# Optimization experiments

Measured on AMD Instinct MI355X. Metric: run time of the kernel, lower is better.

The kernel has to match this reference:

```python
import jax, jax.numpy as jnp
import numpy as np

N_NODES = 100000
N_EDGES = 1600000
N_GRAPHS = 128
CONV = [64, 64, 64]
HID = [256, 128, 2]
GFT = 64
EPS = 1e-5
NEG_SLOPE = 0.01


def leaky_relu(x):
    return jnp.where(x >= 0, x, NEG_SLOPE * x)


def setup_inputs() -> dict:
    key = jax.random.key(0)
    ks = jax.random.split(key, 32)
    inp = {}
    inp['x'] = jax.random.normal(ks[0], (N_NODES, CONV[0]), dtype=jnp.float32)
    inp['edge_index'] = jax.random.randint(ks[1], (2, N_EDGES), 0, N_NODES, dtype=jnp.int64)
    inp['graph_features'] = jax.random.normal(ks[2], (N_GRAPHS, GFT), dtype=jnp.float32)
    inp['batch'] = jnp.sort(jax.random.randint(ks[3], (N_NODES,), 0, N_GRAPHS, dtype=jnp.int64))
    # SAGEConv params per layer: W_l (aggregated branch, with bias), W_r (root branch), BN gamma/beta
    ki = 4
    for li in range(len(CONV) - 1):
        fin, fout = CONV[li], CONV[li + 1]
        s = 1.0 / np.sqrt(fin)
        inp[f'Wl{li}'] = jax.random.uniform(ks[ki], (fin, fout), minval=-s, maxval=s); ki += 1
        inp[f'bl{li}'] = jax.random.uniform(ks[ki], (fout,), minval=-s, maxval=s); ki += 1
        inp[f'Wr{li}'] = jax.random.uniform(ks[ki], (fin, fout), minval=-s, maxval=s); ki += 1
        inp[f'g{li}'] = jnp.ones((fout,), jnp.float32)
        inp[f'b{li}'] = jnp.zeros((fout,), jnp.float32)
    # MLP: Linear(128->256), LeakyReLU, Linear(256->128), LeakyReLU, Linear(128->2)
    dims = [CONV[-1] + GFT] + HID
    for li in range(len(HID)):
        fin, fout = dims[li], dims[li + 1]
        s = 1.0 / np.sqrt(fin)
        inp[f'Wm{li}'] = jax.random.uniform(ks[ki], (fin, fout), minval=-s, maxval=s); ki += 1
        inp[f'bm{li}'] = jax.random.uniform(ks[ki], (fout,), minval=-s, maxval=s); ki += 1
    return inp


def _sage_block(x, src, dst, Wl, bl, Wr, gamma, beta):
    # PyG SAGEConv (aggr='mean'): out = lin_l(mean_{j in N(i)} x_j) + lin_r(x_i)
    msgs = x[src]                                               # [E, Fin] gather
    agg = jax.ops.segment_sum(msgs, dst, num_segments=N_NODES)  # [N, Fin] scatter-add
    deg = jax.ops.segment_sum(jnp.ones((src.shape[0],), x.dtype), dst, num_segments=N_NODES)
    agg = agg / jnp.maximum(deg, 1.0)[:, None]
    h = agg @ Wl + bl + x @ Wr
    h = leaky_relu(h)
    # BatchNorm1d (training mode: batch stats over nodes, biased variance)
    mu = h.mean(axis=0)
    var = h.var(axis=0)
    return (h - mu) * jax.lax.rsqrt(var + EPS) * gamma + beta


def reference(x, edge_index, graph_features, batch,
              Wl0, bl0, Wr0, g0, b0, Wl1, bl1, Wr1, g1, b1,
              Wm0, bm0, Wm1, bm1, Wm2, bm2):
    src, dst = edge_index[0], edge_index[1]
    h = _sage_block(x, src, dst, Wl0, bl0, Wr0, g0, b0)
    h = _sage_block(h, src, dst, Wl1, bl1, Wr1, g1, b1)
    # scatter_mean graph pooling
    pooled = jax.ops.segment_sum(h, batch, num_segments=N_GRAPHS)
    cnt = jax.ops.segment_sum(jnp.ones((h.shape[0],), h.dtype), batch, num_segments=N_GRAPHS)
    pooled = pooled / jnp.maximum(cnt, 1.0)[:, None]
    z = jnp.concatenate([pooled, graph_features], axis=1)       # [G, 128]
    z = leaky_relu(z @ Wm0 + bm0)
    z = leaky_relu(z @ Wm1 + bm1)
    return z @ Wm2 + bm2
```

## Files before the change

kernel.cpp:

```cpp
#include <hip/hip_runtime.h>

#define N_NODES 100000
#define N_EDGES 1600000
#define N_GRAPHS 128
#define FDIM 64
#define EPSV 1e-5f
#define NEG 0.01f

#define NB 782
#define PART_BLOCKS 391
#define CVT_BLOCKS 1563
#define NTILES 6250
#define TPB 8
#define GEMM_BLOCKS 782

typedef short bf16x8 __attribute__((ext_vector_type(8)));
typedef float f32x4  __attribute__((ext_vector_type(4)));

__device__ __forceinline__ float leaky(float x){ return x >= 0.f ? x : NEG*x; }

__device__ __forceinline__ unsigned short f2bf(float x){
    unsigned u = __float_as_uint(x);
    return (unsigned short)((u + 0x7fffu + ((u >> 16) & 1u)) >> 16);
}
__device__ __forceinline__ float bf2f(unsigned short b){
    return __uint_as_float(((unsigned)b) << 16);
}

__global__ __launch_bounds__(256) void k_prep(const float* __restrict__ x,
                                              unsigned short* __restrict__ o,
                                              const int* __restrict__ dst,
                                              int* __restrict__ bhist,
                                              float* __restrict__ bnpart){
    __shared__ int lh[NB];
    int b = blockIdx.x, t = threadIdx.x;
    if (b < CVT_BLOCKS){
        int base = b*1024 + t;
        #pragma unroll
        for (int k2 = 0; k2 < 4; ++k2){
            int i = base + k2*256;
            if (i < (N_NODES*FDIM)/4){
                float4 v = ((const float4*)x)[i];
                ushort4 r;
                r.x = f2bf(v.x); r.y = f2bf(v.y); r.z = f2bf(v.z); r.w = f2bf(v.w);
                ((ushort4*)o)[i] = r;
            }
        }
        if (b < 16) bnpart[(b << 8) + t] = 0.f;
    } else {
        for (int i = t; i < NB; i += 256) lh[i] = 0;
        __syncthreads();
        int base = (b - CVT_BLOCKS) * 4096;
        #pragma unroll
        for (int k = 0; k < 16; ++k){
            int e = base + k*256 + t;
            if (e < N_EDGES) atomicAdd(&lh[dst[e] >> 7], 1);
        }
        __syncthreads();
        for (int i = t; i < NB; i += 256) if (lh[i]) atomicAdd(&bhist[i], lh[i]);
    }
}

__global__ __launch_bounds__(256) void k_bscan(const int* __restrict__ bhist,
                                               int* __restrict__ boff, int* __restrict__ cur){
    __shared__ int lds[256];
    int t = threadIdx.x;
    int base = t*4;
    int v0 = (base+0 < NB) ? bhist[base+0] : 0;
    int v1 = (base+1 < NB) ? bhist[base+1] : 0;
    int v2 = (base+2 < NB) ? bhist[base+2] : 0;
    int v3 = (base+3 < NB) ? bhist[base+3] : 0;
    lds[t] = v0+v1+v2+v3; __syncthreads();
    for (int off = 1; off < 256; off <<= 1){
        int add = (t >= off) ? lds[t-off] : 0; __syncthreads();
        lds[t] += add; __syncthreads();
    }
    int excl = (t > 0) ? lds[t-1] : 0;
    int p0 = excl, p1 = excl+v0, p2 = excl+v0+v1, p3 = excl+v0+v1+v2;
    if (base+0 < NB){ boff[base+0] = p0; cur[base+0] = p0; }
    if (base+1 < NB){ boff[base+1] = p1; cur[base+1] = p1; }
    if (base+2 < NB){ boff[base+2] = p2; cur[base+2] = p2; }
    if (base+3 < NB){ boff[base+3] = p3; cur[base+3] = p3; }
    if (t == 0) boff[NB] = N_EDGES;
}

__global__ __launch_bounds__(256) void k_part(const int* __restrict__ src, const int* __restrict__ dst,
                                              int* __restrict__ cur, int* __restrict__ packed){
    __shared__ int lh[NB];
    __shared__ int lc[NB];
    int t = threadIdx.x;
    for (int i = t; i < NB; i += 256) lh[i] = 0;
    __syncthreads();
    int base = blockIdx.x * 4096;
    int d[16];
    #pragma unroll
    for (int k = 0; k < 16; ++k){
        int e = base + k*256 + t;
        d[k] = (e < N_EDGES) ? dst[e] : -1;
        if (d[k] >= 0) atomicAdd(&lh[d[k] >> 7], 1);
    }
    __syncthreads();
    for (int i = t; i < NB; i += 256) lc[i] = atomicAdd(&cur[i], lh[i]);
    __syncthreads();
    #pragma unroll
    for (int k = 0; k < 16; ++k){
        int e = base + k*256 + t;
        if (e < N_EDGES){
            int b = d[k] >> 7;
            int p = atomicAdd(&lc[b], 1);
            packed[p] = (src[e] << 7) | (d[k] & 127);
        }
    }
}

__global__ __launch_bounds__(256) void k_sort(const int* __restrict__ packed,
                                              const int* __restrict__ boff,
                                              int* __restrict__ rs, int* __restrict__ colb){
    __shared__ int hist[128];
    __shared__ int curs[128];
    int b = blockIdx.x, t = threadIdx.x;
    int e0 = boff[b], e1 = boff[b+1];
    if (t < 128) hist[t] = 0;
    __syncthreads();
    for (int e = e0 + t; e < e1; e += 256)
        atomicAdd(&hist[packed[e] & 127], 1);
    __syncthreads();
    int cnt = (t < 128) ? hist[t] : 0;
    __syncthreads();
    for (int off = 1; off < 128; off <<= 1){
        int add = (t < 128 && t >= off) ? hist[t-off] : 0;
        __syncthreads();
        if (t < 128) hist[t] += add;
        __syncthreads();
    }
    int nbase = b << 7;
    int nloc = min(128, N_NODES - nbase);
    if (t < nloc){
        int excl = hist[t] - cnt;
        rs[nbase + t] = e0 + excl;
        curs[t] = excl;
    }
    __syncthreads();
    for (int e = e0 + t; e < e1; e += 256){
        int v = packed[e];
        int p = atomicAdd(&curs[v & 127], 1);
        colb[e0 + p] = v & 0xFFFFFF80;
    }
    if (b == 0 && t == 0) rs[N_NODES] = N_EDGES;
}

template<int PASS>
__global__ __launch_bounds__(256) void k_agg(
    const unsigned short* __restrict__ xin, const int* __restrict__ rs,
    const int* __restrict__ colb, unsigned short* __restrict__ agg)
{
    int t = threadIdx.x;
    int lane = t & 63;
    int sub = lane >> 3;
    int q   = lane & 7;
    const char* xb = (const char*)xin + (PASS << 6) + (q << 3);
    int wid = (blockIdx.x << 2) + (t >> 6);
    const int nw = gridDim.x << 2;
    for (int n = wid; n < N_NODES; n += nw){
        int e0 = __builtin_amdgcn_readfirstlane(rs[n]);
        int e1 = __builtin_amdgcn_readfirstlane(rs[n+1]);
        float ax=0.f, ay=0.f, az=0.f, aw=0.f;
        for (int e = e0 + sub; e < e1; e += 32){
            {
                uint2 u = *(const uint2*)(xb + colb[e]);
                ax += __uint_as_float(u.x << 16); ay += __uint_as_float(u.x & 0xffff0000u);
                az += __uint_as_float(u.y << 16); aw += __uint_as_float(u.y & 0xffff0000u);
            }
            int i1 = e + 8, i2 = e + 16, i3 = e + 24;
            if (i1 < e1){
                uint2 u = *(const uint2*)(xb + colb[i1]);
                ax += __uint_as_float(u.x << 16); ay += __uint_as_float(u.x & 0xffff0000u);
                az += __uint_as_float(u.y << 16); aw += __uint_as_float(u.y & 0xffff0000u);
            }
            if (i2 < e1){
                uint2 u = *(const uint2*)(xb + colb[i2]);
                ax += __uint_as_float(u.x << 16); ay += __uint_as_float(u.x & 0xffff0000u);
                az += __uint_as_float(u.y << 16); aw += __uint_as_float(u.y & 0xffff0000u);
            }
            if (i3 < e1){
                uint2 u = *(const uint2*)(xb + colb[i3]);
                ax += __uint_as_float(u.x << 16); ay += __uint_as_float(u.x & 0xffff0000u);
                az += __uint_as_float(u.y << 16); aw += __uint_as_float(u.y & 0xffff0000u);
            }
        }
        ax += __shfl_xor(ax, 8, 64); ay += __shfl_xor(ay, 8, 64);
        az += __shfl_xor(az, 8, 64); aw += __shfl_xor(aw, 8, 64);
        ax += __shfl_xor(ax, 16, 64); ay += __shfl_xor(ay, 16, 64);
        az += __shfl_xor(az, 16, 64); aw += __shfl_xor(aw, 16, 64);
        ax += __shfl_xor(ax, 32, 64); ay += __shfl_xor(ay, 32, 64);
        az += __shfl_xor(az, 32, 64); aw += __shfl_xor(aw, 32, 64);
        if (sub == 0){
            float rd = 1.f / fmaxf((float)(e1 - e0), 1.f);
            ushort4 o;
            o.x = f2bf(ax*rd); o.y = f2bf(ay*rd);
            o.z = f2bf(az*rd); o.w = f2bf(aw*rd);
            *(ushort4*)((char*)agg + (((size_t)n) << 7) + (PASS << 6) + (q << 3)) = o;
        }
    }
}

template<bool AFF>
__global__ __launch_bounds__(256) void k_gemm(
    const unsigned short* __restrict__ agg,
    const unsigned short* __restrict__ xin,
    unsigned short* __restrict__ hout,
    const int* __restrict__ rs, const int* __restrict__ batch,
    const float* __restrict__ Wl, const float* __restrict__ Wr,
    const float* __restrict__ scale,
    const float* __restrict__ bbias, const float* __restrict__ bdelta,
    float* __restrict__ bnpart, float* __restrict__ S)
{
    __shared__ float sS[8*64];
    int t = threadIdx.x;
    int lane = t & 63;
    int jt = t >> 6;
    int g = lane >> 4, r = lane & 15;
    int j = (jt << 4) + r;

    bf16x8 wlh[2], wll[2], wrh[2], wrl[2];
    #pragma unroll
    for (int ks = 0; ks < 2; ++ks){
        #pragma unroll
        for (int i = 0; i < 8; ++i){
            int k = (ks << 5) + (g << 3) + i;
            float s = AFF ? scale[k] : 1.f;
            float wv = Wl[(k << 6) + j] * s;
            unsigned u = __float_as_uint(wv);
            wlh[ks][i] = (short)(u >> 16);
            float lf = wv - __uint_as_float(u & 0xffff0000u);
            wll[ks][i] = (short)(__float_as_uint(lf) >> 16);
            wv = Wr[(k << 6) + j] * s;
            u = __float_as_uint(wv);
            wrh[ks][i] = (short)(u >> 16);
            lf = wv - __uint_as_float(u & 0xffff0000u);
            wrl[ks][i] = (short)(__float_as_uint(lf) >> 16);
        }
    }

    float bb = bbias[j];
    float bd = AFF ? bdelta[j] : 0.f;

    int gbase = 0, span = 0;
    if (AFF){
        for (int i = t; i < 512; i += 256) sS[i] = 0.f;
        int nfirst = blockIdx.x * (TPB*16);
        int nlast  = min(nfirst + TPB*16 - 1, N_NODES - 1);
        gbase = batch[nfirst];
        span  = batch[nlast] - gbase + 1;
        __syncthreads();
    }

    float bs = 0.f, bq = 0.f;
    int c0 = blockIdx.x * TPB;
    int cend = min(c0 + TPB, NTILES);

    auto LOADT = [&](int tile, bf16x8* A, bf16x8* X, int4& R, int& R5, int4& B){
        size_t rowoff = (((size_t)((tile << 4) + r)) << 6) + (g << 3);
        const bf16x8* pa = (const bf16x8*)(agg + rowoff);
        const bf16x8* px = (const bf16x8*)(xin + rowoff);
        A[0] = pa[0]; A[1] = pa[4];
        X[0] = px[0]; X[1] = px[4];
        if (AFF){
            int nb = (tile << 4) + (g << 2);
            R  = *(const int4*)(rs + nb);
            R5 = rs[nb + 4];
            B  = *(const int4*)(batch + nb);
        }
    };

    auto POOL = [&](int gr, float hv){
        int lg = gr - gbase;
        if (lg < 8) atomicAdd(&sS[(lg << 6) + j], hv);
        else        atomicAdd(&S[(gr << 6) + j], hv);
    };

    auto COMPUTE = [&](int tile, const bf16x8* A, const bf16x8* X,
                       const int4& R, int R5, const int4& B){
        f32x4 accA = {0.f, 0.f, 0.f, 0.f};
        f32x4 accX = {0.f, 0.f, 0.f, 0.f};
        accA = __builtin_amdgcn_mfma_f32_16x16x32_bf16(A[0], wlh[0], accA, 0, 0, 0);
        accA = __builtin_amdgcn_mfma_f32_16x16x32_bf16(A[0], wll[0], accA, 0, 0, 0);
        accA = __builtin_amdgcn_mfma_f32_16x16x32_bf16(A[1], wlh[1], accA, 0, 0, 0);
        accA = __builtin_amdgcn_mfma_f32_16x16x32_bf16(A[1], wll[1], accA, 0, 0, 0);
        accX = __builtin_amdgcn_mfma_f32_16x16x32_bf16(X[0], wrh[0], accX, 0, 0, 0);
        accX = __builtin_amdgcn_mfma_f32_16x16x32_bf16(X[0], wrl[0], accX, 0, 0, 0);
        accX = __builtin_amdgcn_mfma_f32_16x16x32_bf16(X[1], wrh[1], accX, 0, 0, 0);
        accX = __builtin_amdgcn_mfma_f32_16x16x32_bf16(X[1], wrl[1], accX, 0, 0, 0);

        int nb = (tile << 4) + (g << 2);
        if (AFF){
            float hv;
            hv = accA[0] + accX[0] + bb + ((R.y - R.x) > 0 ? bd : 0.f);
            hv = leaky(hv); bs += hv; bq += hv*hv; POOL(B.x, hv);
            hv = accA[1] + accX[1] + bb + ((R.z - R.y) > 0 ? bd : 0.f);
            hv = leaky(hv); bs += hv; bq += hv*hv; POOL(B.y, hv);
            hv = accA[2] + accX[2] + bb + ((R.w - R.z) > 0 ? bd : 0.f);
            hv = leaky(hv); bs += hv; bq += hv*hv; POOL(B.z, hv);
            hv = accA[3] + accX[3] + bb + ((R5 - R.w) > 0 ? bd : 0.f);
            hv = leaky(hv); bs += hv; bq += hv*hv; POOL(B.w, hv);
        } else {
            #pragma unroll
            for (int q = 0; q < 4; ++q){
                float hv = leaky(accA[q] + accX[q] + bb);
                unsigned short h16 = f2bf(hv);
                float hr = bf2f(h16);
                hout[((size_t)(nb + q) << 6) + j] = h16;
                bs += hr; bq += hr*hr;
            }
        }
    };

    bf16x8 Aa[2], Xa[2], Ab[2], Xb[2];
    int4 Ra = {0,0,0,0}, Rb = {0,0,0,0}, Ba = {0,0,0,0}, Bb = {0,0,0,0};
    int R5a = 0, R5b = 0;

    LOADT(c0, Aa, Xa, Ra, R5a, Ba);
    for (int c = c0; c < cend; c += 2){
        if (c + 1 < cend) LOADT(c + 1, Ab, Xb, Rb, R5b, Bb);
        COMPUTE(c, Aa, Xa, Ra, R5a, Ba);
        if (c + 2 < cend) LOADT(c + 2, Aa, Xa, Ra, R5a, Ba);
        if (c + 1 < cend) COMPUTE(c + 1, Ab, Xb, Rb, R5b, Bb);
    }

    bs += __shfl_xor(bs, 16, 64); bs += __shfl_xor(bs, 32, 64);
    bq += __shfl_xor(bq, 16, 64); bq += __shfl_xor(bq, 32, 64);
    if (lane < 16){
        float* bp = bnpart + ((blockIdx.x & 31) * 128);
        atomicAdd(&bp[(jt << 4) + lane], bs);
        atomicAdd(&bp[64 + (jt << 4) + lane], bq);
    }

    if (AFF){
        __syncthreads();
        int sp = min(span, 8);
        for (int i = t; i < (sp << 6); i += 256){
            float v = sS[i];
            if (v != 0.f) atomicAdd(&S[((gbase + (i >> 6)) << 6) + (i & 63)], v);
        }
    }
}

template<bool FOLD>
__global__ __launch_bounds__(64) void k_bnfin(
    float* __restrict__ bnpart,
    const float* __restrict__ gamma, const float* __restrict__ beta,
    const float* __restrict__ Wl_nx, const float* __restrict__ Wr_nx,
    const float* __restrict__ bl_nx,
    float* __restrict__ scale, float* __restrict__ shift,
    float* __restrict__ bbias, float* __restrict__ bdelta,
    float* __restrict__ Szero)
{
    __shared__ float ssh[64];
    int j = threadIdx.x;
    float s = 0.f, q = 0.f;
    #pragma unroll 8
    for (int i = 0; i < 32; ++i){
        s += bnpart[i*128 + j];
        q += bnpart[i*128 + 64 + j];
    }
    float mu  = s * (1.0f/N_NODES);
    float var = q * (1.0f/N_NODES) - mu*mu;
    float sc  = gamma[j] * rsqrtf(var + EPSV);
    float sh  = beta[j] - mu*sc;
    scale[j] = sc; shift[j] = sh;
    if (FOLD){
        ssh[j] = sh;
        __syncthreads();
        float bbv = bl_nx[j], bdv = 0.f;
        #pragma unroll 8
        for (int k = 0; k < 64; ++k){
            bbv += ssh[k] * Wr_nx[(k << 6) + j];
            bdv += ssh[k] * Wl_nx[(k << 6) + j];
        }
        bbias[j] = bbv; bdelta[j] = bdv;
        __syncthreads();
        for (int i = j; i < 4096; i += 64) bnpart[i] = 0.f;
        for (int i = j; i < N_GRAPHS*FDIM; i += 64) Szero[i] = 0.f;
    }
}

__global__ __launch_bounds__(256) void k_mlp(
    const float* __restrict__ S, const int* __restrict__ batch,
    const float* __restrict__ scale, const float* __restrict__ shift,
    const float* __restrict__ gf,
    const float* __restrict__ Wm0, const float* __restrict__ bm0,
    const float* __restrict__ Wm1, const float* __restrict__ bm1,
    const float* __restrict__ Wm2, const float* __restrict__ bm2,
    float* __restrict__ out)
{
    __shared__ int seg[2];
    __shared__ float z[128];
    __shared__ float h1[256];
    __shared__ float h2[128];
    int g = blockIdx.x, t = threadIdx.x;
    if (t < 2){
        int target = g + t;
        int lo = 0, hi = N_NODES;
        while (lo < hi){ int mid = (lo+hi)>>1; if (batch[mid] < target) lo = mid+1; else hi = mid; }
        seg[t] = lo;
    }
    __syncthreads();
    float cnt = (float)(seg[1] - seg[0]);
    if (t < 64)
        z[t] = (scale[t]*S[(g<<6)+t] + cnt*shift[t]) / fmaxf(cnt, 1.f);
    else if (t < 128)
        z[t] = gf[g*64 + (t-64)];
    __syncthreads();
    float acc = bm0[t];
    #pragma unroll 8
    for (int k = 0; k < 128; ++k) acc += z[k]*Wm0[k*256 + t];
    h1[t] = leaky(acc);
    __syncthreads();
    if (t < 128){
        float a = bm1[t];
        #pragma unroll 8
        for (int k = 0; k < 256; ++k) a += h1[k]*Wm1[k*128 + t];
        h2[t] = leaky(a);
    }
    __syncthreads();
    if (t < 2){
        float a = bm2[t];
        for (int k = 0; k < 128; ++k) a += h2[k]*Wm2[k*2 + t];
        out[g*2 + t] = a;
    }
}

extern "C" void kernel_launch(void* const* d_in, const int* in_sizes, int n_in,
                              void* d_out, int out_size, void* d_ws, size_t ws_size,
                              hipStream_t stream) {
    const float* x     = (const float*)d_in[0];
    const int*   ei    = (const int*)d_in[1];
    const float* gf    = (const float*)d_in[2];
    const int*   batch = (const int*)d_in[3];
    const float* Wl0 = (const float*)d_in[4];
    const float* bl0 = (const float*)d_in[5];
    const float* Wr0 = (const float*)d_in[6];
    const float* g0  = (const float*)d_in[7];
    const float* b0  = (const float*)d_in[8];
    const float* Wl1 = (const float*)d_in[9];
    const float* bl1 = (const float*)d_in[10];
    const float* Wr1 = (const float*)d_in[11];
    const float* g1  = (const float*)d_in[12];
    const float* b1  = (const float*)d_in[13];
    const float* Wm0 = (const float*)d_in[14];
    const float* bm0 = (const float*)d_in[15];
    const float* Wm1 = (const float*)d_in[16];
    const float* bm1 = (const float*)d_in[17];
    const float* Wm2 = (const float*)d_in[18];
    const float* bm2 = (const float*)d_in[19];

    int*   bhist  = (int*)d_ws;
    int*   boff   = bhist + NB;
    int*   cur    = boff + NB + 1;
    int*   packed = (int*)d_ws + 2348;
    int*   rs     = packed + N_EDGES;
    int*   colb   = rs + 100004;
    unsigned short* xbf   = (unsigned short*)(colb + N_EDGES);
    unsigned short* h1bf  = xbf + (size_t)N_NODES*FDIM;
    unsigned short* aggbf = h1bf + (size_t)N_NODES*FDIM;
    float* bnpart = (float*)(aggbf + (size_t)N_NODES*FDIM);
    float* S      = bnpart + 4096;
    float* scale0 = S + N_GRAPHS*FDIM;
    float* shift0 = scale0 + 64;
    float* scale1 = scale0 + 128;
    float* shift1 = scale0 + 192;
    float* bbias  = scale0 + 256;
    float* bdelta = scale0 + 320;

    const int* srcp = ei;
    const int* dstp = ei + N_EDGES;

    hipMemsetAsync(bhist, 0, NB*sizeof(int), stream);
    k_prep<<<CVT_BLOCKS + PART_BLOCKS, 256, 0, stream>>>(x, xbf, dstp, bhist, bnpart);
    k_bscan<<<1, 256, 0, stream>>>(bhist, boff, cur);
    k_part<<<PART_BLOCKS, 256, 0, stream>>>(srcp, dstp, cur, packed);
    k_sort<<<NB, 256, 0, stream>>>(packed, boff, rs, colb);

    k_agg<0><<<2048, 256, 0, stream>>>(xbf, rs, colb, aggbf);
    k_agg<1><<<2048, 256, 0, stream>>>(xbf, rs, colb, aggbf);
    k_gemm<false><<<GEMM_BLOCKS, 256, 0, stream>>>(
        aggbf, xbf, h1bf, rs, batch,
        Wl0, Wr0, nullptr, bl0, nullptr, bnpart, nullptr);
    k_bnfin<true><<<1, 64, 0, stream>>>(bnpart, g0, b0, Wl1, Wr1, bl1,
                                        scale0, shift0, bbias, bdelta, S);

    k_agg<0><<<2048, 256, 0, stream>>>(h1bf, rs, colb, aggbf);
    k_agg<1><<<2048, 256, 0, stream>>>(h1bf, rs, colb, aggbf);
    k_gemm<true><<<GEMM_BLOCKS, 256, 0, stream>>>(
        aggbf, h1bf, nullptr, rs, batch,
        Wl1, Wr1, scale0, bbias, bdelta, bnpart, S);
    k_bnfin<false><<<1, 64, 0, stream>>>(bnpart, g1, b1, nullptr, nullptr, nullptr,
                                         scale1, shift1, nullptr, nullptr, nullptr);

    k_mlp<<<N_GRAPHS, 256, 0, stream>>>(S, batch, scale1, shift1, gf,
                                        Wm0, bm0, Wm1, bm1, Wm2, bm2, (float*)d_out);
}
```

Before: 306.7 us.

## Merge two half-feature aggregation passes into one full-row pass; shrink GEMM tiles per block

The neighbor-aggregation kernel now has each wave cover all 64 features of a node in a single launch, with 16 lanes per row and 4 edges in flight. Previously two launches each covered 32 features. This halves the CSR index reads and the number of launches, at the cost of fewer edges processed in parallel per node. The GEMM now processes 2 tiles per block across 3125 blocks instead of 8 tiles with a software pipeline, and batch-norm partials are spread over 128 atomic slots instead of 32 to reduce contention. The finalize kernel uses 256 threads to clear the larger partial buffer.

```diff
diff --git a/kernel.cpp b/kernel.cpp
--- a/kernel.cpp
+++ b/kernel.cpp
@@ -11,8 +11,9 @@
 #define PART_BLOCKS 391
 #define CVT_BLOCKS 1563
 #define NTILES 6250
-#define TPB 8
-#define GEMM_BLOCKS 782
+#define TPB 2
+#define GEMM_BLOCKS 3125
+#define BN_SLOTS 128
 
 typedef short bf16x8 __attribute__((ext_vector_type(8)));
 typedef float f32x4  __attribute__((ext_vector_type(4)));
@@ -46,7 +47,7 @@
                 ((ushort4*)o)[i] = r;
             }
         }
-        if (b < 16) bnpart[(b << 8) + t] = 0.f;
+        if (b < 64) bnpart[(b << 8) + t] = 0.f;
     } else {
         for (int i = t; i < NB; i += 256) lh[i] = 0;
         __syncthreads();
@@ -149,29 +150,28 @@
     if (b == 0 && t == 0) rs[N_NODES] = N_EDGES;
 }
 
-template<int PASS>
 __global__ __launch_bounds__(256) void k_agg(
     const unsigned short* __restrict__ xin, const int* __restrict__ rs,
     const int* __restrict__ colb, unsigned short* __restrict__ agg)
 {
     int t = threadIdx.x;
     int lane = t & 63;
-    int sub = lane >> 3;
-    int q   = lane & 7;
-    const char* xb = (const char*)xin + (PASS << 6) + (q << 3);
+    int sub = lane >> 4;
+    int q   = lane & 15;
+    const char* xb = (const char*)xin + (q << 3);
     int wid = (blockIdx.x << 2) + (t >> 6);
     const int nw = gridDim.x << 2;
     for (int n = wid; n < N_NODES; n += nw){
         int e0 = __builtin_amdgcn_readfirstlane(rs[n]);
         int e1 = __builtin_amdgcn_readfirstlane(rs[n+1]);
         float ax=0.f, ay=0.f, az=0.f, aw=0.f;
-        for (int e = e0 + sub; e < e1; e += 32){
-            {
-                uint2 u = *(const uint2*)(xb + colb[e]);
+        for (int e = e0; e < e1; e += 16){
+            int i0 = e + sub, i1 = e + 4 + sub, i2 = e + 8 + sub, i3 = e + 12 + sub;
+            if (i0 < e1){
+                uint2 u = *(const uint2*)(xb + colb[i0]);
                 ax += __uint_as_float(u.x << 16); ay += __uint_as_float(u.x & 0xffff0000u);
                 az += __uint_as_float(u.y << 16); aw += __uint_as_float(u.y & 0xffff0000u);
             }
-            int i1 = e + 8, i2 = e + 16, i3 = e + 24;
             if (i1 < e1){
                 uint2 u = *(const uint2*)(xb + colb[i1]);
                 ax += __uint_as_float(u.x << 16); ay += __uint_as_float(u.x & 0xffff0000u);
@@ -188,8 +188,6 @@
                 az += __uint_as_float(u.y << 16); aw += __uint_as_float(u.y & 0xffff0000u);
             }
         }
-        ax += __shfl_xor(ax, 8, 64); ay += __shfl_xor(ay, 8, 64);
-        az += __shfl_xor(az, 8, 64); aw += __shfl_xor(aw, 8, 64);
         ax += __shfl_xor(ax, 16, 64); ay += __shfl_xor(ay, 16, 64);
         az += __shfl_xor(az, 16, 64); aw += __shfl_xor(aw, 16, 64);
         ax += __shfl_xor(ax, 32, 64); ay += __shfl_xor(ay, 32, 64);
@@ -199,7 +197,7 @@
             ushort4 o;
             o.x = f2bf(ax*rd); o.y = f2bf(ay*rd);
             o.z = f2bf(az*rd); o.w = f2bf(aw*rd);
-            *(ushort4*)((char*)agg + (((size_t)n) << 7) + (PASS << 6) + (q << 3)) = o;
+            *(ushort4*)((char*)agg + (((size_t)n) << 7) + (q << 3)) = o;
         }
     }
 }
@@ -257,7 +255,6 @@
 
     float bs = 0.f, bq = 0.f;
     int c0 = blockIdx.x * TPB;
-    int cend = min(c0 + TPB, NTILES);
 
     auto LOADT = [&](int tile, bf16x8* A, bf16x8* X, int4& R, int& R5, int4& B){
         size_t rowoff = (((size_t)((tile << 4) + r)) << 6) + (g << 3);
@@ -319,18 +316,15 @@
     int4 Ra = {0,0,0,0}, Rb = {0,0,0,0}, Ba = {0,0,0,0}, Bb = {0,0,0,0};
     int R5a = 0, R5b = 0;
 
-    LOADT(c0, Aa, Xa, Ra, R5a, Ba);
-    for (int c = c0; c < cend; c += 2){
-        if (c + 1 < cend) LOADT(c + 1, Ab, Xb, Rb, R5b, Bb);
-        COMPUTE(c, Aa, Xa, Ra, R5a, Ba);
-        if (c + 2 < cend) LOADT(c + 2, Aa, Xa, Ra, R5a, Ba);
-        if (c + 1 < cend) COMPUTE(c + 1, Ab, Xb, Rb, R5b, Bb);
-    }
+    LOADT(c0 + 0, Aa, Xa, Ra, R5a, Ba);
+    LOADT(c0 + 1, Ab, Xb, Rb, R5b, Bb);
+    COMPUTE(c0 + 0, Aa, Xa, Ra, R5a, Ba);
+    COMPUTE(c0 + 1, Ab, Xb, Rb, R5b, Bb);
 
     bs += __shfl_xor(bs, 16, 64); bs += __shfl_xor(bs, 32, 64);
     bq += __shfl_xor(bq, 16, 64); bq += __shfl_xor(bq, 32, 64);
     if (lane < 16){
-        float* bp = bnpart + ((blockIdx.x & 31) * 128);
+        float* bp = bnpart + ((blockIdx.x & (BN_SLOTS-1)) * 128);
         atomicAdd(&bp[(jt << 4) + lane], bs);
         atomicAdd(&bp[64 + (jt << 4) + lane], bq);
     }
@@ -346,7 +340,7 @@
 }
 
 template<bool FOLD>
-__global__ __launch_bounds__(64) void k_bnfin(
+__global__ __launch_bounds__(256) void k_bnfin(
     float* __restrict__ bnpart,
     const float* __restrict__ gamma, const float* __restrict__ beta,
     const float* __restrict__ Wl_nx, const float* __restrict__ Wr_nx,
@@ -356,31 +350,37 @@
     float* __restrict__ Szero)
 {
     __shared__ float ssh[64];
-    int j = threadIdx.x;
-    float s = 0.f, q = 0.f;
-    #pragma unroll 8
-    for (int i = 0; i < 32; ++i){
-        s += bnpart[i*128 + j];
-        q += bnpart[i*128 + 64 + j];
-    }
-    float mu  = s * (1.0f/N_NODES);
-    float var = q * (1.0f/N_NODES) - mu*mu;
-    float sc  = gamma[j] * rsqrtf(var + EPSV);
-    float sh  = beta[j] - mu*sc;
-    scale[j] = sc; shift[j] = sh;
+    int t = threadIdx.x;
+    if (t < 64){
+        int j = t;
+        float s = 0.f, q = 0.f;
+        #pragma unroll 8
+        for (int i = 0; i < BN_SLOTS; ++i){
+            s += bnpart[i*128 + j];
+            q += bnpart[i*128 + 64 + j];
+        }
+        float mu  = s * (1.0f/N_NODES);
+        float var = q * (1.0f/N_NODES) - mu*mu;
+        float sc  = gamma[j] * rsqrtf(var + EPSV);
+        float sh  = beta[j] - mu*sc;
+        scale[j] = sc; shift[j] = sh;
+        ssh[j] = sh;
+    }
+    __syncthreads();
     if (FOLD){
-        ssh[j] = sh;
-        __syncthreads();
-        float bbv = bl_nx[j], bdv = 0.f;
-        #pragma unroll 8
-        for (int k = 0; k < 64; ++k){
-            bbv += ssh[k] * Wr_nx[(k << 6) + j];
-            bdv += ssh[k] * Wl_nx[(k << 6) + j];
-        }
-        bbias[j] = bbv; bdelta[j] = bdv;
-        __syncthreads();
-        for (int i = j; i < 4096; i += 64) bnpart[i] = 0.f;
-        for (int i = j; i < N_GRAPHS*FDIM; i += 64) Szero[i] = 0.f;
+        if (t < 64){
+            int j = t;
+            float bbv = bl_nx[j], bdv = 0.f;
+            #pragma unroll 8
+            for (int k = 0; k < 64; ++k){
+                bbv += ssh[k] * Wr_nx[(k << 6) + j];
+                bdv += ssh[k] * Wl_nx[(k << 6) + j];
+            }
+            bbias[j] = bbv; bdelta[j] = bdv;
+        }
+        __syncthreads();
+        for (int i = t; i < BN_SLOTS*128; i += 256) bnpart[i] = 0.f;
+        for (int i = t; i < N_GRAPHS*FDIM; i += 256) Szero[i] = 0.f;
     }
 }
 
@@ -464,7 +464,7 @@
     unsigned short* h1bf  = xbf + (size_t)N_NODES*FDIM;
     unsigned short* aggbf = h1bf + (size_t)N_NODES*FDIM;
     float* bnpart = (float*)(aggbf + (size_t)N_NODES*FDIM);
-    float* S      = bnpart + 4096;
+    float* S      = bnpart + BN_SLOTS*128;
     float* scale0 = S + N_GRAPHS*FDIM;
     float* shift0 = scale0 + 64;
     float* scale1 = scale0 + 128;
@@ -481,21 +481,19 @@
     k_part<<<PART_BLOCKS, 256, 0, stream>>>(srcp, dstp, cur, packed);
     k_sort<<<NB, 256, 0, stream>>>(packed, boff, rs, colb);
 
-    k_agg<0><<<2048, 256, 0, stream>>>(xbf, rs, colb, aggbf);
-    k_agg<1><<<2048, 256, 0, stream>>>(xbf, rs, colb, aggbf);
+    k_agg<<<2048, 256, 0, stream>>>(xbf, rs, colb, aggbf);
     k_gemm<false><<<GEMM_BLOCKS, 256, 0, stream>>>(
         aggbf, xbf, h1bf, rs, batch,
         Wl0, Wr0, nullptr, bl0, nullptr, bnpart, nullptr);
-    k_bnfin<true><<<1, 64, 0, stream>>>(bnpart, g0, b0, Wl1, Wr1, bl1,
-                                        scale0, shift0, bbias, bdelta, S);
-
-    k_agg<0><<<2048, 256, 0, stream>>>(h1bf, rs, colb, aggbf);
-    k_agg<1><<<2048, 256, 0, stream>>>(h1bf, rs, colb, aggbf);
+    k_bnfin<true><<<1, 256, 0, stream>>>(bnpart, g0, b0, Wl1, Wr1, bl1,
+                                         scale0, shift0, bbias, bdelta, S);
+
+    k_agg<<<2048, 256, 0, stream>>>(h1bf, rs, colb, aggbf);
     k_gemm<true><<<GEMM_BLOCKS, 256, 0, stream>>>(
         aggbf, h1bf, nullptr, rs, batch,
         Wl1, Wr1, scale0, bbias, bdelta, bnpart, S);
-    k_bnfin<false><<<1, 64, 0, stream>>>(bnpart, g1, b1, nullptr, nullptr, nullptr,
-                                         scale1, shift1, nullptr, nullptr, nullptr);
+    k_bnfin<false><<<1, 256, 0, stream>>>(bnpart, g1, b1, nullptr, nullptr, nullptr,
+                                          scale1, shift1, nullptr, nullptr, nullptr);
 
     k_mlp<<<N_GRAPHS, 256, 0, stream>>>(S, batch, scale1, shift1, gf,
                                         Wm0, bm0, Wm1, bm1, Wm2, bm2, (float*)d_out);
```

Measured after the change: 283.7 us. -7.5%, faster.
